# Optimization experiments

Measured on AMD Instinct MI355X. Metric: run time of the kernel, lower is better.

The kernel has to match this reference:

```python
import jax, jax.numpy as jnp
import numpy as np

HIDDEN = 1024
HEADS = 16
HEAD_DIM = HIDDEN // HEADS


def setup_inputs() -> dict:
    key = jax.random.key(0)
    ks = jax.random.split(key, 8)
    B, S = 2, 2048
    scale = 1.0 / np.sqrt(HIDDEN)
    inp = {
        "hidden_states": jax.random.normal(ks[0], (B, S, HIDDEN), dtype=jnp.float32),
        "attention_mask": jnp.zeros((B, 1, 1, S), dtype=jnp.float32),
        "q_w": jax.random.normal(ks[1], (HIDDEN, HIDDEN), dtype=jnp.float32) * scale,
        "q_b": jnp.zeros((HIDDEN,), dtype=jnp.float32),
        "k_w": jax.random.normal(ks[2], (HIDDEN, HIDDEN), dtype=jnp.float32) * scale,
        "k_b": jnp.zeros((HIDDEN,), dtype=jnp.float32),
        "v_w": jax.random.normal(ks[3], (HIDDEN, HIDDEN), dtype=jnp.float32) * scale,
        "v_b": jnp.zeros((HIDDEN,), dtype=jnp.float32),
    }
    return inp


def _split_heads(x):
    # [B, S, H] -> [B, heads, S, head_dim]
    B, S, _ = x.shape
    return x.reshape(B, S, HEADS, HEAD_DIM).transpose(0, 2, 1, 3)


def reference(hidden_states, attention_mask, q_w, q_b, k_w, k_b, v_w, v_b):
    # Linear projections (torch Linear: x @ W.T + b; here weights stored as [in, out])
    q = _split_heads(hidden_states @ q_w + q_b)  # [B, h, S, d]
    k = _split_heads(hidden_states @ k_w + k_b)
    v = _split_heads(hidden_states @ v_w + v_b)

    scores = jnp.einsum("bhqd,bhkd->bhqk", q, k) / jnp.sqrt(jnp.float32(HEAD_DIM))
    scores = scores + attention_mask  # additive mask, broadcast [B,1,1,S]
    probs = jax.nn.softmax(scores, axis=-1)
    # dropout prob = 0.0 -> identity
    ctx = jnp.einsum("bhqk,bhkd->bhqd", probs, v)  # [B, h, S, d]
    B, _, S, _ = ctx.shape
    ctx = ctx.transpose(0, 2, 1, 3).reshape(B, S, HIDDEN)
    return ctx
```

## Files before the change

### kernel.cpp

```cpp
#include <hip/hip_runtime.h>

typedef __bf16 bf16;
typedef __attribute__((ext_vector_type(8))) __bf16 bf16x8;
typedef __attribute__((ext_vector_type(4))) __bf16 bf16x4;
typedef __attribute__((ext_vector_type(4))) float f32x4;

#define MFMA(a, b, c) __builtin_amdgcn_mfma_f32_16x16x32_bf16((a), (b), (c), 0, 0, 0)
#define LOG2E 1.44269504088896340736f

__device__ __forceinline__ bf16x8 cvt8(float4 a, float4 b) {
  bf16x8 r;
  r[0] = (bf16)a.x; r[1] = (bf16)a.y; r[2] = (bf16)a.z; r[3] = (bf16)a.w;
  r[4] = (bf16)b.x; r[5] = (bf16)b.y; r[6] = (bf16)b.z; r[7] = (bf16)b.w;
  return r;
}

__device__ __forceinline__ void stage16(const bf16* g, bf16* l) {
  __builtin_amdgcn_global_load_lds(
      (const __attribute__((address_space(1))) void*)g,
      (__attribute__((address_space(3))) void*)l, 16, 0, 0);
}

__global__ __launch_bounds__(256)
void cvt(const float* __restrict__ hs, const float* __restrict__ qw,
         const float* __restrict__ kw, const float* __restrict__ vw,
         bf16* __restrict__ Xb, bf16* __restrict__ Wt) {
  const int bid = blockIdx.x, tid = threadIdx.x;
  if (bid < 2048) {
    size_t off = (size_t)bid * 2048 + tid * 8;
    float4 x0 = *(const float4*)(hs + off);
    float4 x1 = *(const float4*)(hs + off + 4);
    *(bf16x8*)(Xb + off) = cvt8(x0, x1);
  } else {
    int t = bid - 2048;
    int z = t >> 8, ti = t & 255;
    const float* W = (z == 0) ? qw : (z == 1) ? kw : vw;
    int k0 = (ti >> 4) * 64, n0 = (ti & 15) * 64;
    __shared__ bf16 T[64 * 72];
    #pragma unroll
    for (int i = 0; i < 16; ++i) {
      int e = i * 256 + tid;
      int kr = e >> 6, nc = e & 63;
      T[nc * 72 + kr] = (bf16)W[(size_t)(k0 + kr) * 1024 + n0 + nc];
    }
    __syncthreads();
    #pragma unroll
    for (int i = 0; i < 2; ++i) {
      int e = i * 256 + tid;
      int nr = e >> 3, kg = e & 7;
      *(bf16x8*)(Wt + (size_t)z * 1048576 + (size_t)(n0 + nr) * 1024 + k0 + kg * 8) =
          *(const bf16x8*)&T[nr * 72 + kg * 8];
    }
  }
}

__global__ __launch_bounds__(256, 3)
void qkv_gemm(const bf16* __restrict__ Xb, const bf16* __restrict__ Wt,
              const float* __restrict__ qbias, const float* __restrict__ kbias,
              const float* __restrict__ vbias,
              bf16* __restrict__ qo, bf16* __restrict__ ko, bf16* __restrict__ vo) {
  const int blk = blockIdx.x;
  const int xcd = blk & 7, slot = blk >> 3;
  const int mb = xcd * 4 + slot / 24;
  const int nb = slot % 24;
  const int z = nb >> 3, nbm = nb & 7;
  const bf16* W = Wt + (size_t)z * 1048576;

  const int tid = threadIdx.x;
  const int wave = tid >> 6, lane = tid & 63, quad = lane >> 4, c = lane & 15;
  const int wr = wave >> 1, wc = wave & 1;
  const int lrow = lane >> 3;
  const int lg = (lane & 7) ^ lrow;

  __shared__ bf16 As[128 * 64];
  __shared__ bf16 Bs[128 * 64];

  f32x4 acc[4][4] = {};

  for (int k0 = 0; k0 < 1024; k0 += 64) {
    #pragma unroll
    for (int i = 0; i < 4; ++i) {
      int r = wave * 32 + i * 8;
      stage16(Xb + (size_t)(mb * 128 + r + lrow) * 1024 + k0 + lg * 8, &As[r * 64]);
      stage16(W + (size_t)(nbm * 128 + r + lrow) * 1024 + k0 + lg * 8, &Bs[r * 64]);
    }
    __syncthreads();
    #pragma unroll
    for (int ch = 0; ch < 2; ++ch) {
      bf16x8 af[4];
      #pragma unroll
      for (int rt = 0; rt < 4; ++rt) {
        int row = wr * 64 + rt * 16 + c;
        af[rt] = *(const bf16x8*)&As[row * 64 + ((((ch << 2) | quad) ^ (c & 7)) << 3)];
      }
      #pragma unroll
      for (int nt = 0; nt < 4; ++nt) {
        int row = wc * 64 + nt * 16 + c;
        bf16x8 bfrag = *(const bf16x8*)&Bs[row * 64 + ((((ch << 2) | quad) ^ (c & 7)) << 3)];
        #pragma unroll
        for (int rt = 0; rt < 4; ++rt)
          acc[rt][nt] = MFMA(af[rt], bfrag, acc[rt][nt]);
      }
    }
    __syncthreads();
  }

  const float* bias = (z == 0) ? qbias : (z == 1) ? kbias : vbias;
  float bv[4];
  #pragma unroll
  for (int nt = 0; nt < 4; ++nt)
    bv[nt] = bias[nbm * 128 + wc * 64 + nt * 16 + c];

  if (z == 2) {
    #pragma unroll
    for (int rt = 0; rt < 4; ++rt)
      #pragma unroll
      for (int nt = 0; nt < 4; ++nt) {
        int m0 = mb * 128 + wr * 64 + rt * 16 + 4 * quad;
        int n = nbm * 128 + wc * 64 + nt * 16 + c;
        bf16x4 pk;
        #pragma unroll
        for (int reg = 0; reg < 4; ++reg) pk[reg] = (bf16)(acc[rt][nt][reg] + bv[nt]);
        int b = m0 >> 11, s0 = m0 & 2047, h = n >> 6, d = n & 63;
        *(bf16x4*)&vo[(((size_t)b * 16 + h) * 64 + d) * 2048 + s0] = pk;
      }
  } else {
    bf16* dst = (z == 0) ? qo : ko;
    const float scale = (z == 0) ? 0.125f * LOG2E : 1.0f;
    #pragma unroll
    for (int rt = 0; rt < 4; ++rt)
      #pragma unroll
      for (int nt = 0; nt < 4; ++nt)
        #pragma unroll
        for (int reg = 0; reg < 4; ++reg) {
          float v = (acc[rt][nt][reg] + bv[nt]) * scale;
          int m = mb * 128 + wr * 64 + rt * 16 + 4 * quad + reg;
          int n = nbm * 128 + wc * 64 + nt * 16 + c;
          int b = m >> 11, s = m & 2047, h = n >> 6, d = n & 63;
          dst[(((size_t)b * 16 + h) * 2048 + s) * 64 + d] = (bf16)v;
        }
  }
}

__global__ __launch_bounds__(512, 4)
void attn(const bf16* __restrict__ qg, const bf16* __restrict__ kg,
          const bf16* __restrict__ vtg, const float* __restrict__ mask,
          float* __restrict__ out) {
  const int blk = blockIdx.x;
  const int xcd = blk & 7, slot = blk >> 3;
  const int bh = xcd * 4 + (slot >> 4);
  const int qblk = slot & 15;
  const int b = bh >> 4, h = bh & 15;
  const int tid = threadIdx.x;
  const int wave = tid >> 6, lane = tid & 63, quad = lane >> 4, c = lane & 15;
  const int lrow = lane >> 3, lg = (lane & 7) ^ lrow;

  __shared__ bf16 Ks[64 * 64];
  __shared__ bf16 Vs[64 * 64];
  __shared__ bf16 Ps[8][1024];

  const bf16* qb_ = qg + (size_t)bh * 2048 * 64;
  const bf16* kb_ = kg + (size_t)bh * 2048 * 64;
  const bf16* vb_ = vtg + (size_t)bh * 64 * 2048;

  bf16x8 qf[2];
  #pragma unroll
  for (int ch = 0; ch < 2; ++ch)
    qf[ch] = *(const bf16x8*)(qb_ +
        (size_t)(qblk * 128 + wave * 16 + c) * 64 + ch * 32 + quad * 8);

  f32x4 o[4] = {};
  float lsum[4] = {};

  for (int kt = 0; kt < 32; ++kt) {
    {
      int r = wave * 8;
      stage16(kb_ + (size_t)(kt * 64 + r + lrow) * 64 + lg * 8, &Ks[r * 64]);
      stage16(vb_ + (size_t)(r + lrow) * 2048 + kt * 64 + lg * 8, &Vs[r * 64]);
    }
    __syncthreads();

    f32x4 s[4] = {};
    #pragma unroll
    for (int nt = 0; nt < 4; ++nt)
      #pragma unroll
      for (int ch = 0; ch < 2; ++ch) {
        bf16x8 kf = *(const bf16x8*)&Ks[(nt * 16 + c) * 64 +
                                        ((((ch << 2) | quad) ^ (c & 7)) << 3)];
        s[nt] = MFMA(qf[ch], kf, s[nt]);
      }

    float mv[4];
    #pragma unroll
    for (int nt = 0; nt < 4; ++nt)
      mv[nt] = mask[b * 2048 + kt * 64 + nt * 16 + c] * LOG2E;

    #pragma unroll
    for (int nt = 0; nt < 4; ++nt)
      #pragma unroll
      for (int reg = 0; reg < 4; ++reg) {
        float p = __builtin_amdgcn_exp2f(s[nt][reg] + mv[nt]);
        lsum[reg] += p;
        int r = 4 * quad + reg;
        int gk = nt * 2 + (c >> 3);
        Ps[wave][r * 64 + ((gk ^ (r & 7)) << 3) + (c & 7)] = (bf16)p;
      }
    __asm__ volatile("s_waitcnt lgkmcnt(0)" ::: "memory");

    #pragma unroll
    for (int ch = 0; ch < 2; ++ch) {
      bf16x8 pa = *(const bf16x8*)&Ps[wave][c * 64 +
                                           ((((ch << 2) | quad) ^ (c & 7)) << 3)];
      #pragma unroll
      for (int nt = 0; nt < 4; ++nt) {
        bf16x8 vf = *(const bf16x8*)&Vs[(nt * 16 + c) * 64 +
                                        ((((ch << 2) | quad) ^ (c & 7)) << 3)];
        o[nt] = MFMA(pa, vf, o[nt]);
      }
    }
    __syncthreads();
  }

  #pragma unroll
  for (int reg = 0; reg < 4; ++reg) {
    float l = lsum[reg];
    #pragma unroll
    for (int off = 1; off < 16; off <<= 1) l += __shfl_xor(l, off, 64);
    float inv = 1.0f / l;
    int srow = qblk * 128 + wave * 16 + 4 * quad + reg;
    #pragma unroll
    for (int nt = 0; nt < 4; ++nt)
      out[((size_t)b * 2048 + srow) * 1024 + h * 64 + nt * 16 + c] =
          o[nt][reg] * inv;
  }
}

extern "C" void kernel_launch(void* const* d_in, const int* in_sizes, int n_in,
                              void* d_out, int out_size, void* d_ws, size_t ws_size,
                              hipStream_t stream) {
  const float* hs   = (const float*)d_in[0];
  const float* mask = (const float*)d_in[1];
  const float* qw   = (const float*)d_in[2];
  const float* qb   = (const float*)d_in[3];
  const float* kw   = (const float*)d_in[4];
  const float* kb   = (const float*)d_in[5];
  const float* vw   = (const float*)d_in[6];
  const float* vb   = (const float*)d_in[7];
  float* out = (float*)d_out;

  bf16* Xb   = (bf16*)d_ws;
  bf16* Wt   = Xb + (size_t)4096 * 1024;
  bf16* q_ws = Wt + (size_t)3 * 1048576;
  bf16* k_ws = q_ws + (size_t)4096 * 1024;
  bf16* v_ws = k_ws + (size_t)4096 * 1024;

  cvt<<<dim3(2816), 256, 0, stream>>>(hs, qw, kw, vw, Xb, Wt);
  qkv_gemm<<<dim3(768), 256, 0, stream>>>(Xb, Wt, qb, kb, vb, q_ws, k_ws, v_ws);
  attn<<<dim3(512), 512, 0, stream>>>(q_ws, k_ws, v_ws, mask, out);
}
```

Baseline: 172.3 us.

## Double-buffer K/V tiles and transpose MFMA operands for vectorized P and output stores

Adds two-slot LDS buffers for the K and V tiles so the next tile's global-to-LDS copy is issued while the current tile is being computed, and drops one barrier per iteration. It also swaps the MFMA operand order so each lane holds one query row, which allows vectorized bf16x4 writes of P, float4 mask loads, fewer row-sum shuffles, and float4 output stores. The extra LDS raises shared memory per block and may lower occupancy under the launch bound of 4 blocks. The wait on vmcnt(0) at the end of each iteration limits how much of the copy latency can actually be hidden.

```diff
diff --git a/kernel.cpp b/kernel.cpp
--- a/kernel.cpp
+++ b/kernel.cpp
@@ -155,8 +155,8 @@
   const int wave = tid >> 6, lane = tid & 63, quad = lane >> 4, c = lane & 15;
   const int lrow = lane >> 3, lg = (lane & 7) ^ lrow;
 
-  __shared__ bf16 Ks[64 * 64];
-  __shared__ bf16 Vs[64 * 64];
+  __shared__ bf16 Ks[2][64 * 64];
+  __shared__ bf16 Vs[2][64 * 64];
   __shared__ bf16 Ps[8][1024];
 
   const bf16* qb_ = qg + (size_t)bh * 2048 * 64;
@@ -170,41 +170,52 @@
         (size_t)(qblk * 128 + wave * 16 + c) * 64 + ch * 32 + quad * 8);
 
   f32x4 o[4] = {};
-  float lsum[4] = {};
+  float lsum = 0.f;
+
+  {
+    int r = wave * 8;
+    stage16(kb_ + (size_t)(r + lrow) * 64 + lg * 8, &Ks[0][r * 64]);
+    stage16(vb_ + (size_t)(r + lrow) * 2048 + lg * 8, &Vs[0][r * 64]);
+  }
+  __asm__ volatile("s_waitcnt vmcnt(0)" ::: "memory");
+  __builtin_amdgcn_s_barrier();
 
   for (int kt = 0; kt < 32; ++kt) {
-    {
+    const int cur = kt & 1;
+
+    if (kt < 31) {
       int r = wave * 8;
-      stage16(kb_ + (size_t)(kt * 64 + r + lrow) * 64 + lg * 8, &Ks[r * 64]);
-      stage16(vb_ + (size_t)(r + lrow) * 2048 + kt * 64 + lg * 8, &Vs[r * 64]);
-    }
-    __syncthreads();
+      stage16(kb_ + (size_t)((kt + 1) * 64 + r + lrow) * 64 + lg * 8,
+              &Ks[cur ^ 1][r * 64]);
+      stage16(vb_ + (size_t)(r + lrow) * 2048 + (kt + 1) * 64 + lg * 8,
+              &Vs[cur ^ 1][r * 64]);
+    }
+    __builtin_amdgcn_sched_barrier(0);
 
     f32x4 s[4] = {};
     #pragma unroll
     for (int nt = 0; nt < 4; ++nt)
       #pragma unroll
       for (int ch = 0; ch < 2; ++ch) {
-        bf16x8 kf = *(const bf16x8*)&Ks[(nt * 16 + c) * 64 +
-                                        ((((ch << 2) | quad) ^ (c & 7)) << 3)];
-        s[nt] = MFMA(qf[ch], kf, s[nt]);
-      }
-
-    float mv[4];
-    #pragma unroll
-    for (int nt = 0; nt < 4; ++nt)
-      mv[nt] = mask[b * 2048 + kt * 64 + nt * 16 + c] * LOG2E;
-
-    #pragma unroll
-    for (int nt = 0; nt < 4; ++nt)
+        bf16x8 kf = *(const bf16x8*)&Ks[cur][(nt * 16 + c) * 64 +
+                                            ((((ch << 2) | quad) ^ (c & 7)) << 3)];
+        s[nt] = MFMA(kf, qf[ch], s[nt]);
+      }
+
+    #pragma unroll
+    for (int nt = 0; nt < 4; ++nt) {
+      float4 mv = *(const float4*)&mask[b * 2048 + kt * 64 + nt * 16 + 4 * quad];
+      bf16x4 pk;
       #pragma unroll
       for (int reg = 0; reg < 4; ++reg) {
-        float p = __builtin_amdgcn_exp2f(s[nt][reg] + mv[nt]);
-        lsum[reg] += p;
-        int r = 4 * quad + reg;
-        int gk = nt * 2 + (c >> 3);
-        Ps[wave][r * 64 + ((gk ^ (r & 7)) << 3) + (c & 7)] = (bf16)p;
-      }
+        float mreg = (reg == 0) ? mv.x : (reg == 1) ? mv.y : (reg == 2) ? mv.z : mv.w;
+        float p = __builtin_amdgcn_exp2f(s[nt][reg] + mreg * LOG2E);
+        lsum += p;
+        pk[reg] = (bf16)p;
+      }
+      int g = (nt * 2 + (quad >> 1)) ^ (c & 7);
+      *(bf16x4*)&Ps[wave][c * 64 + g * 8 + (quad & 1) * 4] = pk;
+    }
     __asm__ volatile("s_waitcnt lgkmcnt(0)" ::: "memory");
 
     #pragma unroll
@@ -213,25 +224,25 @@
                                            ((((ch << 2) | quad) ^ (c & 7)) << 3)];
       #pragma unroll
       for (int nt = 0; nt < 4; ++nt) {
-        bf16x8 vf = *(const bf16x8*)&Vs[(nt * 16 + c) * 64 +
-                                        ((((ch << 2) | quad) ^ (c & 7)) << 3)];
-        o[nt] = MFMA(pa, vf, o[nt]);
-      }
-    }
-    __syncthreads();
-  }
-
+        bf16x8 vf = *(const bf16x8*)&Vs[cur][(nt * 16 + c) * 64 +
+                                            ((((ch << 2) | quad) ^ (c & 7)) << 3)];
+        o[nt] = MFMA(vf, pa, o[nt]);
+      }
+    }
+
+    __asm__ volatile("s_waitcnt vmcnt(0) lgkmcnt(0)" ::: "memory");
+    __builtin_amdgcn_s_barrier();
+  }
+
+  lsum += __shfl_xor(lsum, 16, 64);
+  lsum += __shfl_xor(lsum, 32, 64);
+  const float inv = 1.0f / lsum;
+
+  const int srow = qblk * 128 + wave * 16 + c;
   #pragma unroll
-  for (int reg = 0; reg < 4; ++reg) {
-    float l = lsum[reg];
-    #pragma unroll
-    for (int off = 1; off < 16; off <<= 1) l += __shfl_xor(l, off, 64);
-    float inv = 1.0f / l;
-    int srow = qblk * 128 + wave * 16 + 4 * quad + reg;
-    #pragma unroll
-    for (int nt = 0; nt < 4; ++nt)
-      out[((size_t)b * 2048 + srow) * 1024 + h * 64 + nt * 16 + c] =
-          o[nt][reg] * inv;
+  for (int nt = 0; nt < 4; ++nt) {
+    float4 st = { o[nt][0] * inv, o[nt][1] * inv, o[nt][2] * inv, o[nt][3] * inv };
+    *(float4*)&out[((size_t)b * 2048 + srow) * 1024 + h * 64 + nt * 16 + 4 * quad] = st;
   }
 }
 
```

New measurement: 177.0 us. +2.8%, slower.
